# Kernel tuning notes

Hardware: AMD Instinct MI355X
Metric: run time of the kernel (lower is better)

Reference implementation:

```python
import jax, jax.numpy as jnp
import numpy as np

SELF_DIM = 36
ENT_DIM = 28
HID = 256


def setup_inputs() -> dict:
    key = jax.random.key(0)
    ks = jax.random.split(key, 12)
    B, agent_num, n_noisy = 32768, 20, 20
    obs_dim = SELF_DIM + ENT_DIM * (2 * agent_num - 1 + n_noisy)
    s = 0.02
    return {
        "x": jax.random.normal(ks[0], (B, obs_dim), dtype=jnp.float32),
        "Watt": jax.random.normal(ks[1], (ENT_DIM + SELF_DIM, 1), jnp.float32) * s,
        "batt": jnp.zeros((1,), jnp.float32),
        "We": jax.random.normal(ks[2], (ENT_DIM + SELF_DIM, HID), jnp.float32) * s,
        "be": jnp.zeros((HID,), jnp.float32),
        "Wse": jax.random.normal(ks[3], (2 * SELF_DIM, HID), jnp.float32) * s,
        "bse": jnp.zeros((HID,), jnp.float32),
        "Wg": jax.random.normal(ks[4], (3 * HID, 3), jnp.float32) * s,
        "bg": jnp.zeros((3,), jnp.float32),
        "Wo": jax.random.normal(ks[5], (2 * HID, HID), jnp.float32) * s,
        "bo": jnp.zeros((HID,), jnp.float32),
        "agent_num": agent_num,
    }


def reference(x, Watt, batt, We, be, Wse, bse, Wg, bg, Wo, bo, agent_num):
    B = x.shape[0]
    self_info = x[:, :SELF_DIM]  # [B,36]
    opp_end = SELF_DIM + ENT_DIM * agent_num
    par_end = opp_end + ENT_DIM * (agent_num - 1)
    opps = x[:, SELF_DIM:opp_end].reshape(B, agent_num, ENT_DIM)
    pars = x[:, opp_end:par_end].reshape(B, agent_num - 1, ENT_DIM)
    noisy = x[:, par_end:].reshape(B, -1, ENT_DIM)

    def pool(ent):
        # additive-attention pooling over one entity group
        n = ent.shape[1]
        os_ = jnp.concatenate(
            [jnp.broadcast_to(self_info[:, None, :], (B, n, SELF_DIM)), ent], axis=2
        )  # [B,n,64]
        att = jax.nn.softmax(os_ @ Watt + batt, axis=1)  # [B,n,1]
        es = os_ @ We + be  # [B,n,H]
        return jnp.sum(att * es, axis=1)  # [B,H]

    opp_e, par_e, noi_e = pool(opps), pool(pars), pool(noisy)
    group_e = jnp.stack([opp_e, par_e, noi_e], axis=1)  # [B,3,H]
    gw = jax.nn.softmax(
        jnp.concatenate([opp_e, par_e, noi_e], axis=1) @ Wg + bg, axis=1
    )  # [B,3]
    other = jnp.einsum("bg,bgh->bh", gw, group_e)  # [B,H]
    self_e = jnp.concatenate([self_info, self_info], axis=1) @ Wse + bse  # [B,H]
    obs_embedding = jnp.concatenate([other, self_e], axis=1)  # [B,2H]
    return obs_embedding @ Wo + bo
```

## Files before the change

### kernel.cpp

```cpp
#include <hip/hip_runtime.h>
#include <hip/hip_bf16.h>

#define SELF_D 36
#define ENT_D  28
#define HID    256
#define OBS    1688
#define NWAVES 8192
#define ETS    61

#define WS_A     0
#define WS_B     9216
#define WS_C     16384
#define WS_MSEL  16640
#define WS_MENT  16748
#define WS_CG    17000
#define WS_WATT  17008
#define WS_AT    17040
#define WS_BT    26256
#define WS_TOTAL 33424

__global__ __launch_bounds__(256)
void setup_kernel(const float* __restrict__ Watt, const float* __restrict__ We,
                  const float* __restrict__ be,  const float* __restrict__ Wse,
                  const float* __restrict__ bse, const float* __restrict__ Wg,
                  const float* __restrict__ bg,  const float* __restrict__ Wo,
                  const float* __restrict__ bo,  float* __restrict__ ws) {
  const int blk = blockIdx.x;
  const int c = threadIdx.x;
  if (blk < 36) {
    int k = blk;
    float acc = 0.f;
    for (int r = 0; r < 256; ++r) acc += We[k*256 + r] * Wo[r*256 + c];
    for (int r = 0; r < 256; ++r) acc += (Wse[k*256 + r] + Wse[(36+k)*256 + r]) * Wo[(256+r)*256 + c];
    ws[WS_A + k*256 + c] = acc;
    ws[WS_AT + c*36 + k] = acc;
  } else if (blk < 64) {
    int k = blk - 36;
    float acc = 0.f;
    for (int r = 0; r < 256; ++r) acc += We[(36+k)*256 + r] * Wo[r*256 + c];
    ws[WS_B + k*256 + c] = acc;
    ws[WS_BT + c*28 + k] = acc;
  } else if (blk == 64) {
    float acc = bo[c];
    for (int r = 0; r < 256; ++r) acc += be[r] * Wo[r*256 + c];
    for (int r = 0; r < 256; ++r) acc += bse[r] * Wo[(256+r)*256 + c];
    ws[WS_C + c] = acc;
  } else {
    for (int t = c; t < 391; t += 256) {
      if (t < 108) {
        int k = t / 3, j = t - 3*k;
        float acc = 0.f;
        for (int r = 0; r < 256; ++r) {
          float wg = Wg[r*3 + j] + Wg[(256+r)*3 + j] + Wg[(512+r)*3 + j];
          acc += We[k*256 + r] * wg;
        }
        ws[WS_MSEL + t] = acc;
      } else if (t < 360) {
        int idx = t - 108;
        int g = idx / 84, rem = idx - 84*g;
        int k = rem / 3, j = rem - 3*k;
        float acc = 0.f;
        for (int r = 0; r < 256; ++r) acc += We[(36+k)*256 + r] * Wg[(256*g + r)*3 + j];
        ws[WS_MENT + idx] = acc;
      } else if (t < 363) {
        int j = t - 360;
        float acc = bg[j];
        for (int r = 0; r < 256; ++r)
          acc += be[r] * (Wg[r*3 + j] + Wg[(256+r)*3 + j] + Wg[(512+r)*3 + j]);
        ws[WS_CG + j] = acc;
      } else {
        int k = t - 363;
        ws[WS_WATT + k] = Watt[36 + k];
      }
    }
  }
}

__global__ __launch_bounds__(256)
void pool_kernel(const float* __restrict__ x, const float* __restrict__ ws,
                 float* __restrict__ out, int B) {
  __shared__ __align__(16) float ET[4][28*ETS + 4];
  __shared__ __align__(16) float sself[4][40];
  __shared__ __align__(16) float satt[4][64];
  __shared__ __align__(16) float sebar[4][88];
  __shared__ __align__(16) float sM[360];

  const int tid = threadIdx.x;
  const int w = tid >> 6, ln = tid & 63;

  for (int t = tid; t < 360; t += 256) sM[t] = ws[WS_MSEL + t];
  if (ln < 28) ET[w][ln*ETS + 39] = 0.f;
  __syncthreads();

  const float* Wp = ws + WS_WATT;
  const float cg0 = ws[WS_CG + 0], cg1 = ws[WS_CG + 1], cg2 = ws[WS_CG + 2];

  int  eoff[7];
  bool went[7];
#pragma unroll
  for (int i = 0; i < 7; ++i) {
    int q = i*64 + ln;
    went[i] = (q >= 9) && (q < 422);
    int e = (q - 9) / 7, t = (q - 9) % 7;
    int s = e + (e >= 39 ? 1 : 0);
    eoff[i] = t*4*ETS + s;
  }
  const bool wself0 = (ln < 9);

  const bool lval = (ln < 60) && (ln != 39);
  const int  lcol = lval ? ln : 0;

  const int  mg0 = ln / 28, mk0 = ln - 28*mg0;
  const int  base0 = mk0*ETS + mg0*20;
  const bool mv1 = (ln < 20);
  const int  base1 = (ln + 8)*ETS + 40;

  const int  gj = ln >> 4, gch = ln & 15;
  const bool gact = (gj < 3) && (gch < 15);

  const int row0 = blockIdx.x * 4 + w;

  float4 pf[7];
  if (row0 < B) {
    const float4* xr = (const float4*)(x + (size_t)row0 * OBS);
#pragma unroll
    for (int i = 0; i < 7; ++i) { int idx = i*64 + ln; if (idx < 422) pf[i] = xr[idx]; }
  }

  for (int row = row0; row < B; row += NWAVES) {
    if (wself0) *(float4*)&sself[w][ln*4] = pf[0];
#pragma unroll
    for (int i = 0; i < 7; ++i) {
      if (went[i]) {
        float* p = &ET[w][eoff[i]];
        p[0]     = pf[i].x;
        p[ETS]   = pf[i].y;
        p[2*ETS] = pf[i].z;
        p[3*ETS] = pf[i].w;
      }
    }

    {
      int nr = row + NWAVES;
      if (nr < B) {
        const float4* xn = (const float4*)(x + (size_t)nr * OBS);
#pragma unroll
        for (int i = 0; i < 7; ++i) { int idx = i*64 + ln; if (idx < 422) pf[i] = xn[idx]; }
      }
    }
    asm volatile("" ::: "memory");

    float l = -1e30f;
    {
      const float* cb = &ET[w][lcol];
      float acc = 0.f;
#pragma unroll
      for (int k = 0; k < 28; ++k) acc += cb[k*ETS] * Wp[k];
      if (lval) l = acc;
    }
    float m = l;
#pragma unroll
    for (int off = 32; off; off >>= 1) m = fmaxf(m, __shfl_xor(m, off));
    satt[w][ln] = lval ? __expf(l - m) : 0.f;
    asm volatile("" ::: "memory");

    {
      const float* vb = &ET[w][base0];
      const float* pa = &satt[w][mg0 * 20];
      float us = 0.f, uv = 0.f;
#pragma unroll
      for (int i = 0; i < 20; ++i) { float pp = pa[i]; us += pp; uv += pp * vb[i]; }
      sebar[w][ln] = uv / us;
    }
    if (mv1) {
      const float* vb = &ET[w][base1];
      const float* pa = &satt[w][40];
      float us = 0.f, uv = 0.f;
#pragma unroll
      for (int i = 0; i < 20; ++i) { float pp = pa[i]; us += pp; uv += pp * vb[i]; }
      sebar[w][ln + 64] = uv / us;
    }
    asm volatile("" ::: "memory");

    float gl = 0.f;
    if (gact) {
#pragma unroll
      for (int q = 0; q < 8; ++q) {
        int c = q*15 + gch;
        float v = (c < SELF_D) ? sself[w][c] : sebar[w][c - SELF_D];
        gl += v * sM[c*3 + gj];
      }
    }
#pragma unroll
    for (int off = 1; off < 16; off <<= 1) gl += __shfl_xor(gl, off);
    float l0 = __shfl(gl, 0)  + cg0;
    float l1 = __shfl(gl, 16) + cg1;
    float l2 = __shfl(gl, 32) + cg2;
    float mm = fmaxf(l0, fmaxf(l1, l2));
    float e0x = __expf(l0 - mm), e1x = __expf(l1 - mm), e2x = __expf(l2 - mm);
    float inv = 1.f / (e0x + e1x + e2x);

    float fv;
    if (ln < SELF_D) {
      fv = sself[w][ln];
    } else {
      int k = ln - SELF_D;
      fv = (e0x * sebar[w][k] + e1x * sebar[w][28 + k] + e2x * sebar[w][56 + k]) * inv;
    }
    out[(size_t)row * HID + ln] = fv;
  }
}

#define PR_ROWS 32
#define PR_CH   8
__global__ __launch_bounds__(256)
void proj_kernel(const float* __restrict__ ws, float* __restrict__ out) {
  __shared__ __align__(16) float sf[PR_CH][64];
  const int tid = threadIdx.x;

  float4 Av[9], Bv[7];
#pragma unroll
  for (int q = 0; q < 9; ++q) Av[q] = ((const float4*)(ws + WS_AT + tid * 36))[q];
#pragma unroll
  for (int q = 0; q < 7; ++q) Bv[q] = ((const float4*)(ws + WS_BT + tid * 28))[q];
  const float cc = ws[WS_C + tid];

  const size_t row0 = (size_t)blockIdx.x * PR_ROWS;
  for (int chk = 0; chk < PR_ROWS / PR_CH; ++chk) {
    const size_t rbase = row0 + chk * PR_CH;
    if (tid < PR_CH * 16) {
      int r = tid >> 4, q = tid & 15;
      ((float4*)&sf[r][0])[q] = ((const float4*)(out + (rbase + r) * HID))[q];
    }
    __syncthreads();
#pragma unroll
    for (int r = 0; r < PR_CH; ++r) {
      float acc = cc;
      const float4* f4 = (const float4*)&sf[r][0];
#pragma unroll
      for (int q = 0; q < 9; ++q) {
        float4 s = f4[q];
        acc += Av[q].x*s.x + Av[q].y*s.y + Av[q].z*s.z + Av[q].w*s.w;
      }
#pragma unroll
      for (int q = 0; q < 7; ++q) {
        float4 s = f4[9 + q];
        acc += Bv[q].x*s.x + Bv[q].y*s.y + Bv[q].z*s.z + Bv[q].w*s.w;
      }
      out[(rbase + r) * HID + tid] = acc;
    }
    __syncthreads();
  }
}

extern "C" void kernel_launch(void* const* d_in, const int* in_sizes, int n_in,
                              void* d_out, int out_size, void* d_ws, size_t ws_size,
                              hipStream_t stream) {
  const float* x    = (const float*)d_in[0];
  const float* Watt = (const float*)d_in[1];
  const float* We   = (const float*)d_in[3];
  const float* be   = (const float*)d_in[4];
  const float* Wse  = (const float*)d_in[5];
  const float* bse  = (const float*)d_in[6];
  const float* Wg   = (const float*)d_in[7];
  const float* bg   = (const float*)d_in[8];
  const float* Wo   = (const float*)d_in[9];
  const float* bo   = (const float*)d_in[10];
  float* out = (float*)d_out;
  float* ws  = (float*)d_ws;
  const int B = in_sizes[0] / OBS;

  setup_kernel<<<66, 256, 0, stream>>>(Watt, We, be, Wse, bse, Wg, bg, Wo, bo, ws);
  pool_kernel<<<NWAVES / 4, 256, 0, stream>>>(x, ws, out, B);
  proj_kernel<<<B / PR_ROWS, 256, 0, stream>>>(ws, out);
}
```

Measured before the change: 106.9 us.

## Store entity tile as bf16 and normalize attention via lane permutes

```diff
diff --git a/kernel.cpp b/kernel.cpp
--- a/kernel.cpp
+++ b/kernel.cpp
@@ -6,7 +6,6 @@
 #define HID    256
 #define OBS    1688
 #define NWAVES 8192
-#define ETS    61
 
 #define WS_A     0
 #define WS_B     9216
@@ -76,47 +75,70 @@
   }
 }
 
+__device__ __forceinline__ unsigned pack_bf2(float a, float b) {
+  unsigned ua = __float_as_uint(a);
+  unsigned ub = __float_as_uint(b);
+  ua = (ua + 0x7fffu + ((ua >> 16) & 1u)) >> 16;
+  ub = (ub + 0x7fffu + ((ub >> 16) & 1u)) & 0xffff0000u;
+  return ua | ub;
+}
+__device__ __forceinline__ float bf_lo(unsigned u) { return __uint_as_float(u << 16); }
+__device__ __forceinline__ float bf_hi(unsigned u) { return __uint_as_float(u & 0xffff0000u); }
+__device__ __forceinline__ float bperm(int idx4, float v) {
+  return __int_as_float(__builtin_amdgcn_ds_bpermute(idx4, __float_as_int(v)));
+}
+
 __global__ __launch_bounds__(256)
 void pool_kernel(const float* __restrict__ x, const float* __restrict__ ws,
                  float* __restrict__ out, int B) {
-  __shared__ __align__(16) float ET[4][28*ETS + 4];
+  __shared__ __align__(16) unsigned short tileh[4][60*28];
   __shared__ __align__(16) float sself[4][40];
-  __shared__ __align__(16) float satt[4][64];
   __shared__ __align__(16) float sebar[4][88];
-  __shared__ __align__(16) float sM[360];
 
   const int tid = threadIdx.x;
   const int w = tid >> 6, ln = tid & 63;
 
-  for (int t = tid; t < 360; t += 256) sM[t] = ws[WS_MSEL + t];
-  if (ln < 28) ET[w][ln*ETS + 39] = 0.f;
-  __syncthreads();
+  if (ln < 7) ((uint2*)&tileh[w][39*28])[ln] = make_uint2(0u, 0u);
 
   const float* Wp = ws + WS_WATT;
   const float cg0 = ws[WS_CG + 0], cg1 = ws[WS_CG + 1], cg2 = ws[WS_CG + 2];
 
-  int  eoff[7];
-  bool went[7];
+  int  soff[7]; bool went[7];
 #pragma unroll
   for (int i = 0; i < 7; ++i) {
     int q = i*64 + ln;
-    went[i] = (q >= 9) && (q < 422);
-    int e = (q - 9) / 7, t = (q - 9) % 7;
+    bool v = (q >= 9) && (q < 422);
+    went[i] = v;
+    int qm = v ? (q - 9) : 0;
+    int e = qm / 7, t = qm - 7*e;
     int s = e + (e >= 39 ? 1 : 0);
-    eoff[i] = t*4*ETS + s;
-  }
-  const bool wself0 = (ln < 9);
+    soff[i] = s*28 + 4*t;
+  }
+  const bool wself = (ln < 9);
 
   const bool lval = (ln < 60) && (ln != 39);
-  const int  lcol = lval ? ln : 0;
-
-  const int  mg0 = ln / 28, mk0 = ln - 28*mg0;
-  const int  base0 = mk0*ETS + mg0*20;
-  const bool mv1 = (ln < 20);
-  const int  base1 = (ln + 8)*ETS + 40;
+  const int  lrow = (ln < 60 ? ln : 0) * 28;
+
+  int rotb[5];
+  {
+    int base = (ln < 60) ? (ln/20)*20 : 60;
+    int n    = (ln < 60) ? 20 : 4;
+    int off  = ln - base;
+    const int rs[5] = {1, 2, 4, 8, 16};
+#pragma unroll
+    for (int j = 0; j < 5; ++j) rotb[j] = (base + (off + rs[j]) % n) * 4;
+  }
+
+  const bool mact = (ln < 21);
+  const int  mg = ln / 7, mkq = ln - 7*mg;
+  const int  mrow0 = (mg*20)*28 + 4*mkq;
 
   const int  gj = ln >> 4, gch = ln & 15;
   const bool gact = (gj < 3) && (gch < 15);
+  float gw8[8];
+#pragma unroll
+  for (int q = 0; q < 8; ++q)
+    gw8[q] = gact ? ws[WS_MSEL + (q*15 + gch)*3 + gj] : 0.f;
 
   const int row0 = blockIdx.x * 4 + w;
 
@@ -128,15 +150,12 @@
   }
 
   for (int row = row0; row < B; row += NWAVES) {
-    if (wself0) *(float4*)&sself[w][ln*4] = pf[0];
+    if (wself) *(float4*)&sself[w][ln*4] = pf[0];
 #pragma unroll
     for (int i = 0; i < 7; ++i) {
       if (went[i]) {
-        float* p = &ET[w][eoff[i]];
-        p[0]     = pf[i].x;
-        p[ETS]   = pf[i].y;
-        p[2*ETS] = pf[i].z;
-        p[3*ETS] = pf[i].w;
+        uint2 u = make_uint2(pack_bf2(pf[i].x, pf[i].y), pack_bf2(pf[i].z, pf[i].w));
+        *(uint2*)&tileh[w][soff[i]] = u;
       }
     }
 
@@ -150,35 +169,50 @@
     }
     asm volatile("" ::: "memory");
 
+    float4 ev[7];
     float l = -1e30f;
     {
-      const float* cb = &ET[w][lcol];
       float acc = 0.f;
 #pragma unroll
-      for (int k = 0; k < 28; ++k) acc += cb[k*ETS] * Wp[k];
+      for (int t = 0; t < 7; ++t) {
+        uint2 u = *(const uint2*)&tileh[w][lrow + 4*t];
+        ev[t].x = bf_lo(u.x); ev[t].y = bf_hi(u.x);
+        ev[t].z = bf_lo(u.y); ev[t].w = bf_hi(u.y);
+        acc += ev[t].x*Wp[4*t] + ev[t].y*Wp[4*t+1] + ev[t].z*Wp[4*t+2] + ev[t].w*Wp[4*t+3];
+      }
       if (lval) l = acc;
     }
+
     float m = l;
 #pragma unroll
     for (int off = 32; off; off >>= 1) m = fmaxf(m, __shfl_xor(m, off));
-    satt[w][ln] = lval ? __expf(l - m) : 0.f;
+    float a = lval ? __expf(l - m) : 0.f;
+    float w2  = a  + bperm(rotb[0], a);
+    float w4  = w2 + bperm(rotb[1], w2);
+    float w8  = w4 + bperm(rotb[2], w4);
+    float w16 = w8 + bperm(rotb[3], w8);
+    float us  = w16 + bperm(rotb[4], w4);
+    float an  = a / us;
+
+    if (ln < 60) {
+#pragma unroll
+      for (int t = 0; t < 7; ++t) {
+        uint2 u = make_uint2(pack_bf2(ev[t].x*an, ev[t].y*an),
+                             pack_bf2(ev[t].z*an, ev[t].w*an));
+        *(uint2*)&tileh[w][lrow + 4*t] = u;
+      }
+    }
     asm volatile("" ::: "memory");
 
-    {
-      const float* vb = &ET[w][base0];
-      const float* pa = &satt[w][mg0 * 20];
-      float us = 0.f, uv = 0.f;
-#pragma unroll
-      for (int i = 0; i < 20; ++i) { float pp = pa[i]; us += pp; uv += pp * vb[i]; }
-      sebar[w][ln] = uv / us;
-    }
-    if (mv1) {
-      const float* vb = &ET[w][base1];
-      const float* pa = &satt[w][40];
-      float us = 0.f, uv = 0.f;
-#pragma unroll
-      for (int i = 0; i < 20; ++i) { float pp = pa[i]; us += pp; uv += pp * vb[i]; }
-      sebar[w][ln + 64] = uv / us;
+    if (mact) {
+      float s0 = 0.f, s1 = 0.f, s2 = 0.f, s3 = 0.f;
+#pragma unroll
+      for (int i = 0; i < 20; ++i) {
+        uint2 u = *(const uint2*)&tileh[w][mrow0 + i*28];
+        s0 += bf_lo(u.x); s1 += bf_hi(u.x);
+        s2 += bf_lo(u.y); s3 += bf_hi(u.y);
+      }
+      *(float4*)&sebar[w][mg*28 + 4*mkq] = make_float4(s0, s1, s2, s3);
     }
     asm volatile("" ::: "memory");
 
@@ -188,7 +222,7 @@
       for (int q = 0; q < 8; ++q) {
         int c = q*15 + gch;
         float v = (c < SELF_D) ? sself[w][c] : sebar[w][c - SELF_D];
-        gl += v * sM[c*3 + gj];
+        gl += v * gw8[q];
       }
     }
 #pragma unroll
```

New measurement: 112.2 us. 1.05x slower.
